# Kernel tuning notes

Measured on AMD Instinct MI355X. Metric: run time of the kernel, lower is better.

The kernel has to match this reference:

```python
import jax, jax.numpy as jnp
import numpy as np

B, C, H, W = 16, 384, 56, 56
NH, WS, SS = 12, 7, 3          # num_heads, window_size, shift_size
MLP = 4 * C
N = WS * WS                     # tokens per window (49)
nHW = H // WS                   # windows per side (8)
nW = nHW * nHW                  # windows per image (64)
HD = C // NH                    # head dim (32)
EPS = 1e-5


def _ln(x, g, b):
    mu = jnp.mean(x, axis=-1, keepdims=True)
    var = jnp.mean(jnp.square(x - mu), axis=-1, keepdims=True)
    return (x - mu) * jax.lax.rsqrt(var + EPS) * g + b


def _attn_mask():
    # static shifted-window mask, computed once with numpy (constants)
    img = np.zeros((H, W))
    sl = (slice(0, -WS), slice(-WS, -SS), slice(-SS, None))
    cnt = 0
    for hs in sl:
        for ws_ in sl:
            img[hs, ws_] = cnt
            cnt += 1
    mw = img.reshape(nHW, WS, nHW, WS).transpose(0, 2, 1, 3).reshape(-1, N)
    d = mw[:, None, :] - mw[:, :, None]          # (nW, N, N)
    return jnp.asarray(np.where(d != 0, -100.0, 0.0), jnp.float32)

_MASK = _attn_mask()


def setup_inputs() -> dict:
    key = jax.random.key(0)
    ks = jax.random.split(key, 6)
    rn = lambda k, s: jax.random.normal(k, s, jnp.float32) * 0.02
    return {
        "x": jax.random.normal(ks[0], (B, C, H, W), jnp.float32),
        "norm1_g": jnp.ones((C,), jnp.float32),
        "norm1_b": jnp.zeros((C,), jnp.float32),
        "qkv_w": rn(ks[1], (C, 3 * C)),
        "qkv_b": jnp.zeros((3 * C,), jnp.float32),
        "proj_w": rn(ks[2], (C, C)),
        "proj_b": jnp.zeros((C,), jnp.float32),
        "norm2_g": jnp.ones((C,), jnp.float32),
        "norm2_b": jnp.zeros((C,), jnp.float32),
        "fc1_w": rn(ks[3], (C, MLP)),
        "fc1_b": jnp.zeros((MLP,), jnp.float32),
        "fc2_w": rn(ks[4], (MLP, C)),
        "fc2_b": jnp.zeros((C,), jnp.float32),
    }


def reference(x, norm1_g, norm1_b, qkv_w, qkv_b, proj_w, proj_b,
              norm2_g, norm2_b, fc1_w, fc1_b, fc2_w, fc2_b):
    shortcut = x                                   # (B, C, H, W)
    xh = jnp.transpose(x, (0, 2, 3, 1))            # (B, H, W, C)
    xh = _ln(xh, norm1_g, norm1_b)
    # H, W divisible by WS -> padding is a no-op; shifted window path
    xs = jnp.roll(xh, (-SS, -SS), axis=(1, 2))
    # window partition -> (B*nW, N, C)
    xw = xs.reshape(B, nHW, WS, nHW, WS, C).transpose(0, 1, 3, 2, 4, 5)
    xw = xw.reshape(-1, N, C)
    # attention
    qkv = (xw @ qkv_w + qkv_b).reshape(-1, N, 3, NH, HD).transpose(2, 0, 3, 1, 4)
    q, k, v = qkv[0] * HD ** -0.5, qkv[1], qkv[2]  # (B*nW, NH, N, HD)
    attn = jnp.einsum('whnd,whmd->whnm', q, k)     # (B*nW, NH, N, N)
    attn = attn.reshape(B, nW, NH, N, N) + _MASK[None, :, None]
    attn = jax.nn.softmax(attn, axis=-1).reshape(-1, NH, N, N)
    out = jnp.einsum('whnm,whmd->whnd', attn, v)   # (B*nW, NH, N, HD)
    out = out.transpose(0, 2, 1, 3).reshape(-1, N, C)
    out = out @ proj_w + proj_b
    # window reverse -> (B, H, W, C), un-shift
    xs = out.reshape(B, nHW, nHW, WS, WS, C).transpose(0, 1, 3, 2, 4, 5)
    xs = xs.reshape(B, H, W, C)
    xh = jnp.roll(xs, (SS, SS), axis=(1, 2))
    x2 = shortcut + jnp.transpose(xh, (0, 3, 1, 2))
    # MLP residual (in BHWC)
    xh2 = jnp.transpose(x2, (0, 2, 3, 1))
    h = jax.nn.gelu(_ln(xh2, norm2_g, norm2_b) @ fc1_w + fc1_b,
                    approximate=False) @ fc2_w + fc2_b
    xh2 = xh2 + h
    return jnp.transpose(xh2, (0, 3, 1, 2))
```

## Files before the change

### kernel.cpp

```cpp
#include <hip/hip_runtime.h>
#include <hip/hip_bf16.h>
#include <math.h>
#include <stdint.h>

#define C_ 384
#define TOKENS 50176

typedef __bf16 bf16;
typedef __bf16 bf16x8 __attribute__((ext_vector_type(8)));
typedef __bf16 bf16x4 __attribute__((ext_vector_type(4)));
typedef float  f32x4  __attribute__((ext_vector_type(4)));

__device__ __forceinline__ float b2f(bf16 x) { return (float)x; }
__device__ __forceinline__ bf16  f2b(float x) { return (bf16)x; }

__device__ __forceinline__ float fast_gelu(float v) {
    float u2 = v * fmaf(v * v, 0.07135481f, 1.5957691f);
    return v / (1.0f + __expf(-u2));
}

__device__ __forceinline__ void gld_lds16(const bf16* g, bf16* l) {
    __builtin_amdgcn_global_load_lds(
        (const __attribute__((address_space(1))) void*)g,
        (__attribute__((address_space(3))) void*)l, 16, 0, 0);
}

#define SB() __builtin_amdgcn_sched_barrier(0)
#define SYNC_FENCE() do { __builtin_amdgcn_sched_barrier(0); \
                          __builtin_amdgcn_s_barrier(); \
                          __builtin_amdgcn_sched_barrier(0); } while (0)
#define WAITVM(N) do { asm volatile("s_waitcnt vmcnt(" #N ")" ::: "memory"); SB(); } while (0)
#define WAITLG()  do { asm volatile("s_waitcnt lgkmcnt(0)" ::: "memory"); SB(); } while (0)

__global__ void wtrans_kernel(const float* __restrict__ in, bf16* __restrict__ out,
                              int K, int N) {
    int idx = blockIdx.x * 256 + threadIdx.x;
    if (idx >= K * N) return;
    int n = idx / K, k = idx % K;
    out[idx] = f2b(in[(size_t)k * N + n]);
}

__global__ __launch_bounds__(256) void ln1_gather_kernel(
    const float* __restrict__ x, const float* __restrict__ g,
    const float* __restrict__ bt, bf16* __restrict__ xw) {
    int wave = threadIdx.x >> 6, lane = threadIdx.x & 63;
    int T = blockIdx.x * 4 + wave;
    int wi = T / 49, n = T % 49;
    int b = wi >> 6, w64 = wi & 63;
    int bh = w64 >> 3, bw = w64 & 7;
    int hs = bh * 7 + n / 7 + 3; if (hs >= 56) hs -= 56;
    int wsd = bw * 7 + n % 7 + 3; if (wsd >= 56) wsd -= 56;
    const float* xp = x + (size_t)b * C_ * 3136 + hs * 56 + wsd;
    float v[6];
    #pragma unroll
    for (int k = 0; k < 6; k++) v[k] = xp[(size_t)(lane + k * 64) * 3136];
    float s = v[0] + v[1] + v[2] + v[3] + v[4] + v[5];
    #pragma unroll
    for (int m = 32; m; m >>= 1) s += __shfl_xor(s, m);
    float mu = s * (1.0f / 384.0f);
    float s2 = 0.f;
    #pragma unroll
    for (int k = 0; k < 6; k++) { float d = v[k] - mu; s2 += d * d; }
    #pragma unroll
    for (int m = 32; m; m >>= 1) s2 += __shfl_xor(s2, m);
    float rstd = rsqrtf(s2 * (1.0f / 384.0f) + 1e-5f);
    bf16* op = xw + (size_t)T * 384;
    #pragma unroll
    for (int k = 0; k < 6; k++) {
        int c = lane + k * 64;
        op[c] = f2b((v[k] - mu) * rstd * g[c] + bt[c]);
    }
}

enum { EPI_NONE = 0, EPI_GELU = 1, EPI_PROJ = 2, EPI_FC2 = 3 };


__device__ __forceinline__ void ldg_a2(f32x4& d0, f32x4& d1, const bf16* p) {
    asm volatile("global_load_dwordx4 %0, %2, off\n\t"
                 "global_load_dwordx4 %1, %2, off offset:64"
                 : "=&v"(d0), "=&v"(d1) : "v"(p) : "memory");
}

__device__ __forceinline__ void stage_B(const bf16* const (&gB)[4], bf16* Bsb,
                                        int t, int k0) {
    #pragma unroll
    for (int p = 0; p < 4; p++) gld_lds16(gB[p] + k0, Bsb + (p * 256 + t) * 8);
}

#define LDA(A0, A1)                                                     \
    do {                                                                \
        _Pragma("unroll")                                               \
        for (int i_ = 0; i_ < 4; i_++) ldg_a2(A0[i_], A1[i_], ga[i_]);  \
        _Pragma("unroll")                                               \
        for (int i_ = 0; i_ < 4; i_++) ga[i_] += 64;                    \
    } while (0)

#define RDB(Bsb)                                                              \
    do {                                                                      \
        const char* Bb_ = (const char*)(Bsb);                                 \
        _Pragma("unroll")                                                     \
        for (int j_ = 0; j_ < 4; j_++)                                        \
            b0[j_] = *(const bf16x8*)(Bb_ + bB + j_ * 2048);                  \
        _Pragma("unroll")                                                     \
        for (int j_ = 0; j_ < 4; j_++)                                        \
            b1[j_] = *(const bf16x8*)(Bb_ + (bB ^ 64) + j_ * 2048);           \
    } while (0)

#define MMAC(A0, A1)                                                           \
    do {                                                                       \
        __builtin_amdgcn_s_setprio(1);                                         \
        _Pragma("unroll")                                                      \
        for (int j_ = 0; j_ < 4; j_++)                                         \
            _Pragma("unroll")                                                  \
            for (int i_ = 0; i_ < 4; i_++)                                     \
                acc[j_][i_] = __builtin_amdgcn_mfma_f32_16x16x32_bf16(         \
                    b0[j_], __builtin_bit_cast(bf16x8, A0[i_]), acc[j_][i_],   \
                    0, 0, 0);                                                  \
        _Pragma("unroll")                                                      \
        for (int j_ = 0; j_ < 4; j_++)                                         \
            _Pragma("unroll")                                                  \
            for (int i_ = 0; i_ < 4; i_++)                                     \
                acc[j_][i_] = __builtin_amdgcn_mfma_f32_16x16x32_bf16(         \
                    b1[j_], __builtin_bit_cast(bf16x8, A1[i_]), acc[j_][i_],   \
                    0, 0, 0);                                                  \
        __builtin_amdgcn_s_setprio(0);                                         \
        __builtin_amdgcn_sched_barrier(0);                                     \
    } while (0)

template <int EPI>
__global__ __launch_bounds__(256, 2) void gemm_kernel(
    const bf16* __restrict__ A, const bf16* __restrict__ Wt,
    const float* __restrict__ bias, bf16* __restrict__ Cout,
    int Kdim, int Ndim,
    const float* __restrict__ resx,
    const bf16* __restrict__ resb) {
    __shared__ __align__(16) bf16 Bs[2][128 * 64];
    int t = threadIdx.x;

    int nwg = gridDim.x * gridDim.y;
    int bid = blockIdx.y * gridDim.x + blockIdx.x;
    int q8 = nwg >> 3, r8 = nwg & 7, xcd = bid & 7, off = bid >> 3;
    int swz = (xcd < r8 ? xcd * (q8 + 1) : r8 * (q8 + 1) + (xcd - r8) * q8) + off;
    int n0 = (swz % gridDim.x) * 128;
    int m0 = (swz / gridDim.x) * 128;

    int lane = t & 63, wave = t >> 6;
    int wr = wave >> 1, wc = wave & 1;
    int quad = lane >> 4, lm = lane & 15;
    f32x4 acc[4][4] = {};

    const bf16* gB[4];
    #pragma unroll
    for (int p = 0; p < 4; p++) {
        int idx = p * 256 + t;
        int row = idx >> 3, g = idx & 7;
        int gs = g ^ (row & 7);
        gB[p] = Wt + (size_t)(n0 + row) * Kdim + gs * 8;
    }
    int g0 = quad ^ (lm & 7);
    int bB = ((wc * 64 + lm) * 64 + g0 * 8) * 2;

    const bf16* ga[4];
    #pragma unroll
    for (int i = 0; i < 4; i++)
        ga[i] = A + (size_t)(m0 + wr * 64 + i * 16 + lm) * Kdim + quad * 8;

    f32x4 aE0[4], aE1[4], aO0[4], aO1[4];
    bf16x8 b0[4], b1[4];

    int nt = Kdim >> 6;
    stage_B(gB, Bs[0], t, 0);
    stage_B(gB, Bs[1], t, 64);
    LDA(aE0, aE1);
    WAITVM(0);
    SYNC_FENCE();

    for (int tk = 0; tk < nt; tk += 2) {
        RDB(Bs[0]);
        LDA(aO0, aO1);
        WAITVM(12);
        WAITLG();
        MMAC(aE0, aE1);
        SYNC_FENCE();
        if (tk + 2 < nt) {
            stage_B(gB, Bs[0], t, (tk + 2) << 6);
            WAITVM(12);
        } else {
            WAITVM(8);
        }
        SYNC_FENCE();
        RDB(Bs[1]);
        if (tk + 2 < nt) {
            LDA(aE0, aE1);
            WAITVM(12);
        } else {
            WAITVM(0);
        }
        WAITLG();
        MMAC(aO0, aO1);
        if (tk + 2 < nt) {
            SYNC_FENCE();
            stage_B(gB, Bs[1], t, (tk + 3) << 6);
            WAITVM(12);
            SYNC_FENCE();
        }
    }

    #pragma unroll
    for (int i = 0; i < 4; i++) {
        int m = m0 + wr * 64 + i * 16 + lm;
        size_t resbase = 0;
        if (EPI == EPI_PROJ) {
            int wi = m / 49, n_ = m % 49;
            int b = wi >> 6, w64 = wi & 63;
            int bh = w64 >> 3, bw = w64 & 7;
            int hs = bh * 7 + n_ / 7 + 3; if (hs >= 56) hs -= 56;
            int wsd = bw * 7 + n_ % 7 + 3; if (wsd >= 56) wsd -= 56;
            resbase = (size_t)b * C_ * 3136 + hs * 56 + wsd;
        }
        #pragma unroll
        for (int j = 0; j < 4; j++) {
            int nb = n0 + wc * 64 + j * 16 + quad * 4;
            f32x4 bj = *(const f32x4*)(bias + nb);
            f32x4 v;
            #pragma unroll
            for (int r = 0; r < 4; r++) v[r] = acc[j][i][r] + bj[r];
            if (EPI == EPI_GELU) {
                #pragma unroll
                for (int r = 0; r < 4; r++) v[r] = fast_gelu(v[r]);
            }
            if (EPI == EPI_PROJ) {
                #pragma unroll
                for (int r = 0; r < 4; r++) v[r] += resx[resbase + (size_t)(nb + r) * 3136];
            }
            if (EPI == EPI_FC2) {
                bf16x4 rb = *(const bf16x4*)(resb + (size_t)m * 384 + nb);
                #pragma unroll
                for (int r = 0; r < 4; r++) v[r] += b2f(rb[r]);
            }
            bf16x4 o;
            #pragma unroll
            for (int r = 0; r < 4; r++) o[r] = f2b(v[r]);
            *(bf16x4*)(Cout + (size_t)m * Ndim + nb) = o;
        }
    }
}

__global__ __launch_bounds__(64) void attn_mfma_kernel(const bf16* __restrict__ qkv,
                                                       bf16* __restrict__ aout) {
    __shared__ __align__(16) bf16 pbuf[64 * 72];
    __shared__ int reg_[64];
    int l = threadIdx.x;
    int wi = blockIdx.x / 12, h = blockIdx.x % 12;
    int i16 = l & 15, quad = l >> 4;

    {
        int tok = l < 49 ? l : 48;
        int w64 = wi & 63;
        int bh = w64 >> 3, bw = w64 & 7;
        int hh = bh * 7 + tok / 7, ww = bw * 7 + tok % 7;
        int fh = hh < 49 ? 0 : (hh < 53 ? 1 : 2);
        int fw = ww < 49 ? 0 : (ww < 53 ? 1 : 2);
        reg_[l] = fh * 3 + fw;
    }
    __syncthreads();

    const bf16* qbase = qkv + (size_t)wi * 49 * 1152 + h * 32;

    f32x4 s_[4][4] = {};
    bf16x8 af[4], bfr[4];
    #pragma unroll
    for (int mi = 0; mi < 4; mi++) {
        int m = mi * 16 + i16; if (m > 48) m = 48;
        af[mi] = *(const bf16x8*)(qbase + (size_t)m * 1152 + quad * 8);
    }
    #pragma unroll
    for (int nt = 0; nt < 4; nt++) {
        int n = nt * 16 + i16; if (n > 48) n = 48;
        bfr[nt] = *(const bf16x8*)(qbase + 384 + (size_t)n * 1152 + quad * 8);
    }
    #pragma unroll
    for (int mi = 0; mi < 4; mi++)
        #pragma unroll
        for (int nt = 0; nt < 4; nt++)
            s_[mi][nt] = __builtin_amdgcn_mfma_f32_16x16x32_bf16(af[mi], bfr[nt], s_[mi][nt], 0, 0, 0);

    int creg[4];
    #pragma unroll
    for (int nt = 0; nt < 4; nt++) {
        int c = nt * 16 + i16; if (c > 48) c = 48;
        creg[nt] = reg_[c];
    }

    const float scale = 0.17677669529663687f;
    #pragma unroll
    for (int mi = 0; mi < 4; mi++) {
        #pragma unroll
        for (int r = 0; r < 4; r++) {
            int row = mi * 16 + quad * 4 + r;
            int rreg = reg_[row];
            float v[4]; float mx = -1e30f;
            #pragma unroll
            for (int nt = 0; nt < 4; nt++) {
                int c = nt * 16 + i16;
                float x = s_[mi][nt][r] * scale;
                if (c > 48) x = -1e30f;
                else if (rreg != creg[nt]) x -= 100.0f;
                v[nt] = x; mx = fmaxf(mx, x);
            }
            #pragma unroll
            for (int m = 8; m; m >>= 1) mx = fmaxf(mx, __shfl_xor(mx, m));
            float sum = 0.f;
            #pragma unroll
            for (int nt = 0; nt < 4; nt++) { v[nt] = __expf(v[nt] - mx); sum += v[nt]; }
            #pragma unroll
            for (int m = 8; m; m >>= 1) sum += __shfl_xor(sum, m);
            float inv = 1.0f / sum;
            #pragma unroll
            for (int nt = 0; nt < 4; nt++)
                pbuf[row * 72 + nt * 16 + i16] = f2b(v[nt] * inv);
        }
    }
    __syncthreads();

    f32x4 o_[4][2] = {};
    const bf16* vbase = qkv + (size_t)wi * 49 * 1152 + 768 + h * 32;
    #pragma unroll
    for (int ks = 0; ks < 2; ks++) {
        bf16x8 pa[4];
        #pragma unroll
        for (int mi = 0; mi < 4; mi++)
            pa[mi] = *(const bf16x8*)(pbuf + (mi * 16 + i16) * 72 + ks * 32 + quad * 8);
        bf16x8 vb[2];
        #pragma unroll
        for (int nt = 0; nt < 2; nt++)
            #pragma unroll
            for (int j = 0; j < 8; j++) {
                int tok = ks * 32 + quad * 8 + j; if (tok > 48) tok = 48;
                vb[nt][j] = vbase[(size_t)tok * 1152 + nt * 16 + i16];
            }
        #pragma unroll
        for (int mi = 0; mi < 4; mi++)
            #pragma unroll
            for (int nt = 0; nt < 2; nt++)
                o_[mi][nt] = __builtin_amdgcn_mfma_f32_16x16x32_bf16(pa[mi], vb[nt], o_[mi][nt], 0, 0, 0);
    }

    bf16* obase = aout + (size_t)wi * 49 * 384 + h * 32;
    #pragma unroll
    for (int mi = 0; mi < 4; mi++)
        #pragma unroll
        for (int r = 0; r < 4; r++) {
            int row = mi * 16 + quad * 4 + r;
            if (row < 49) {
                #pragma unroll
                for (int nt = 0; nt < 2; nt++)
                    obase[(size_t)row * 384 + nt * 16 + i16] = f2b(o_[mi][nt][r]);
            }
        }
}

__global__ __launch_bounds__(256) void ln2_kernel(const bf16* __restrict__ x2,
                                                  const float* __restrict__ g,
                                                  const float* __restrict__ bt,
                                                  bf16* __restrict__ x2n) {
    int wave = threadIdx.x >> 6, lane = threadIdx.x & 63;
    int T = blockIdx.x * 4 + wave;
    const bf16* xp = x2 + (size_t)T * 384;
    float v[6];
    #pragma unroll
    for (int k = 0; k < 6; k++) v[k] = b2f(xp[lane + k * 64]);
    float s = v[0] + v[1] + v[2] + v[3] + v[4] + v[5];
    #pragma unroll
    for (int m = 32; m; m >>= 1) s += __shfl_xor(s, m);
    float mu = s * (1.0f / 384.0f);
    float s2 = 0.f;
    #pragma unroll
    for (int k = 0; k < 6; k++) { float d = v[k] - mu; s2 += d * d; }
    #pragma unroll
    for (int m = 32; m; m >>= 1) s2 += __shfl_xor(s2, m);
    float rstd = rsqrtf(s2 * (1.0f / 384.0f) + 1e-5f);
    bf16* op = x2n + (size_t)T * 384;
    #pragma unroll
    for (int k = 0; k < 6; k++) {
        int c = lane + k * 64;
        op[c] = f2b((v[k] - mu) * rstd * g[c] + bt[c]);
    }
}

__global__ __launch_bounds__(256) void untile_kernel(const bf16* __restrict__ otok,
                                                     float* __restrict__ out) {
    __shared__ float tile[56 * 65];
    int t = threadIdx.x;
    int b = blockIdx.x / 336;
    int rem = blockIdx.x % 336;
    int h = rem / 6;
    int c0 = (rem % 6) * 64;
    int hs = h + 53; if (hs >= 56) hs -= 56;
    int bh = hs / 7, th = hs % 7;
    #pragma unroll
    for (int pass = 0; pass < 14; pass++) {
        int w = pass * 4 + (t >> 6);
        int c = t & 63;
        int wsd = w + 53; if (wsd >= 56) wsd -= 56;
        int T = (b * 64 + bh * 8 + wsd / 7) * 49 + th * 7 + wsd % 7;
        tile[w * 65 + c] = b2f(otok[(size_t)T * 384 + c0 + c]);
    }
    __syncthreads();
    #pragma unroll
    for (int pass = 0; pass < 14; pass++) {
        int idx = pass * 256 + t;
        int c = idx / 56, w = idx % 56;
        out[((size_t)(b * 384 + c0 + c)) * 3136 + h * 56 + w] = tile[w * 65 + c];
    }
}

extern "C" void kernel_launch(void* const* d_in, const int* in_sizes, int n_in,
                              void* d_out, int out_size, void* d_ws, size_t ws_size,
                              hipStream_t stream) {
    (void)in_sizes; (void)n_in; (void)out_size; (void)ws_size;
    const float* x      = (const float*)d_in[0];
    const float* n1g    = (const float*)d_in[1];
    const float* n1b    = (const float*)d_in[2];
    const float* qkv_w  = (const float*)d_in[3];
    const float* qkv_b  = (const float*)d_in[4];
    const float* proj_w = (const float*)d_in[5];
    const float* proj_b = (const float*)d_in[6];
    const float* n2g    = (const float*)d_in[7];
    const float* n2b    = (const float*)d_in[8];
    const float* fc1_w  = (const float*)d_in[9];
    const float* fc1_b  = (const float*)d_in[10];
    const float* fc2_w  = (const float*)d_in[11];
    const float* fc2_b  = (const float*)d_in[12];
    float* out = (float*)d_out;
    char* ws = (char*)d_ws;

    bf16* qkv_wT = (bf16*)(ws + 0);
    bf16* proj_wT = (bf16*)(ws + 884736);
    bf16* fc1_wT = (bf16*)(ws + 1179648);
    bf16* fc2_wT = (bf16*)(ws + 2359296);
    bf16* xw   = (bf16*)(ws + 4194304);
    bf16* qkvb = (bf16*)(ws + 42729472);
    bf16* attn = (bf16*)(ws + 158334976);
    bf16* x2   = (bf16*)(ws + 4194304);
    bf16* x2n  = (bf16*)(ws + 42729472);
    bf16* h1   = (bf16*)(ws + 81264640);
    bf16* otok = (bf16*)(ws + 235405312);

    wtrans_kernel<<<(384 * 1152 + 255) / 256, 256, 0, stream>>>(qkv_w, qkv_wT, 384, 1152);
    wtrans_kernel<<<(384 * 384 + 255) / 256, 256, 0, stream>>>(proj_w, proj_wT, 384, 384);
    wtrans_kernel<<<(384 * 1536 + 255) / 256, 256, 0, stream>>>(fc1_w, fc1_wT, 384, 1536);
    wtrans_kernel<<<(1536 * 384 + 255) / 256, 256, 0, stream>>>(fc2_w, fc2_wT, 1536, 384);

    ln1_gather_kernel<<<TOKENS / 4, 256, 0, stream>>>(x, n1g, n1b, xw);

    gemm_kernel<EPI_NONE><<<dim3(9, 392), 256, 0, stream>>>(
        xw, qkv_wT, qkv_b, qkvb, 384, 1152, nullptr, nullptr);

    attn_mfma_kernel<<<12288, 64, 0, stream>>>(qkvb, attn);

    gemm_kernel<EPI_PROJ><<<dim3(3, 392), 256, 0, stream>>>(
        attn, proj_wT, proj_b, x2, 384, 384, x, nullptr);

    ln2_kernel<<<TOKENS / 4, 256, 0, stream>>>(x2, n2g, n2b, x2n);

    gemm_kernel<EPI_GELU><<<dim3(12, 392), 256, 0, stream>>>(
        x2n, fc1_wT, fc1_b, h1, 384, 1536, nullptr, nullptr);

    gemm_kernel<EPI_FC2><<<dim3(3, 392), 256, 0, stream>>>(
        h1, fc2_wT, fc2_b, otok, 1536, 384, nullptr, x2);

    untile_kernel<<<16 * 336, 256, 0, stream>>>(otok, out);
}
```

Baseline: 794.6 us.

## Preload full K weight panel into LDS and double M tile per block

The GEMM kernel now uses 512 threads and a 256-row M tile. For K=384 GEMMs it loads the entire 128x384 weight panel into LDS once with an XOR swizzle and drops the per-iteration double-buffered staging and its barriers. For the K=1536 FC2 GEMM it skips LDS entirely and streams B fragments directly from global memory into registers. This is meant to remove LDS sync overhead and improve reuse, at the cost of 96KB LDS per block (which may limit occupancy) and more register pressure.

Result: slower. 956.0 us (+20.3%).

```diff
diff --git a/kernel.cpp b/kernel.cpp
--- a/kernel.cpp
+++ b/kernel.cpp
@@ -75,35 +75,46 @@
 enum { EPI_NONE = 0, EPI_GELU = 1, EPI_PROJ = 2, EPI_FC2 = 3 };
 
 
-__device__ __forceinline__ void ldg_a2(f32x4& d0, f32x4& d1, const bf16* p) {
+__device__ __forceinline__ void ldg2(f32x4& d0, f32x4& d1, const bf16* p) {
     asm volatile("global_load_dwordx4 %0, %2, off\n\t"
                  "global_load_dwordx4 %1, %2, off offset:64"
                  : "=&v"(d0), "=&v"(d1) : "v"(p) : "memory");
 }
 
-__device__ __forceinline__ void stage_B(const bf16* const (&gB)[4], bf16* Bsb,
-                                        int t, int k0) {
-    #pragma unroll
-    for (int p = 0; p < 4; p++) gld_lds16(gB[p] + k0, Bsb + (p * 256 + t) * 8);
-}
-
 #define LDA(A0, A1)                                                     \
     do {                                                                \
         _Pragma("unroll")                                               \
-        for (int i_ = 0; i_ < 4; i_++) ldg_a2(A0[i_], A1[i_], ga[i_]);  \
+        for (int i_ = 0; i_ < 4; i_++) ldg2(A0[i_], A1[i_], ga[i_]);    \
         _Pragma("unroll")                                               \
         for (int i_ = 0; i_ < 4; i_++) ga[i_] += 64;                    \
     } while (0)
 
-#define RDB(Bsb)                                                              \
+#define LDB(B0, B1)                                                     \
+    do {                                                                \
+        _Pragma("unroll")                                               \
+        for (int j_ = 0; j_ < 4; j_++) ldg2(B0[j_], B1[j_], gb[j_]);    \
+        _Pragma("unroll")                                               \
+        for (int j_ = 0; j_ < 4; j_++) gb[j_] += 64;                    \
+    } while (0)
+
+#define RDBL(TK)                                                              \
     do {                                                                      \
-        const char* Bb_ = (const char*)(Bsb);                                 \
+        const char* wb_ = (const char*)Ws + (TK) * 128;                       \
         _Pragma("unroll")                                                     \
         for (int j_ = 0; j_ < 4; j_++)                                        \
-            b0[j_] = *(const bf16x8*)(Bb_ + bB + j_ * 2048);                  \
+            b0[j_] = *(const bf16x8*)(wb_ + bB + j_ * 12288);                 \
         _Pragma("unroll")                                                     \
         for (int j_ = 0; j_ < 4; j_++)                                        \
-            b1[j_] = *(const bf16x8*)(Bb_ + (bB ^ 64) + j_ * 2048);           \
+            b1[j_] = *(const bf16x8*)(wb_ + (bB ^ 64) + j_ * 12288);          \
+    } while (0)
+
+#define CVTB(BS0, BS1)                                                        \
+    do {                                                                      \
+        _Pragma("unroll")                                                     \
+        for (int j_ = 0; j_ < 4; j_++) {                                      \
+            b0[j_] = __builtin_bit_cast(bf16x8, BS0[j_]);                     \
+            b1[j_] = __builtin_bit_cast(bf16x8, BS1[j_]);                     \
+        }                                                                     \
     } while (0)
 
 #define MMAC(A0, A1)                                                           \
@@ -127,14 +138,14 @@
         __builtin_amdgcn_sched_barrier(0);                                     \
     } while (0)
 
-template <int EPI>
-__global__ __launch_bounds__(256, 2) void gemm_kernel(
+template <int EPI, bool BLDS>
+__global__ __launch_bounds__(512, 2) void gemm_kernel(
     const bf16* __restrict__ A, const bf16* __restrict__ Wt,
     const float* __restrict__ bias, bf16* __restrict__ Cout,
     int Kdim, int Ndim,
     const float* __restrict__ resx,
     const bf16* __restrict__ resb) {
-    __shared__ __align__(16) bf16 Bs[2][128 * 64];
+    __shared__ __align__(16) bf16 Ws[BLDS ? 128 * 384 : 8];
     int t = threadIdx.x;
 
     int nwg = gridDim.x * gridDim.y;
@@ -142,68 +153,75 @@
     int q8 = nwg >> 3, r8 = nwg & 7, xcd = bid & 7, off = bid >> 3;
     int swz = (xcd < r8 ? xcd * (q8 + 1) : r8 * (q8 + 1) + (xcd - r8) * q8) + off;
     int n0 = (swz % gridDim.x) * 128;
-    int m0 = (swz / gridDim.x) * 128;
+    int m0 = (swz / gridDim.x) * 256;
 
     int lane = t & 63, wave = t >> 6;
     int wr = wave >> 1, wc = wave & 1;
     int quad = lane >> 4, lm = lane & 15;
     f32x4 acc[4][4] = {};
 
-    const bf16* gB[4];
-    #pragma unroll
-    for (int p = 0; p < 4; p++) {
-        int idx = p * 256 + t;
-        int row = idx >> 3, g = idx & 7;
-        int gs = g ^ (row & 7);
-        gB[p] = Wt + (size_t)(n0 + row) * Kdim + gs * 8;
-    }
-    int g0 = quad ^ (lm & 7);
-    int bB = ((wc * 64 + lm) * 64 + g0 * 8) * 2;
+    if (BLDS) {
+        #pragma unroll
+        for (int q = 0; q < 12; q++) {
+            int idx = q * 512 + t;
+            int row = idx / 48, cg = idx % 48;
+            int sg = (cg & ~7) | ((cg & 7) ^ (row & 7));
+            gld_lds16(Wt + (size_t)(n0 + row) * 384 + sg * 8, Ws + idx * 8);
+        }
+    }
 
     const bf16* ga[4];
     #pragma unroll
     for (int i = 0; i < 4; i++)
         ga[i] = A + (size_t)(m0 + wr * 64 + i * 16 + lm) * Kdim + quad * 8;
+    const bf16* gb[4];
+    if (!BLDS) {
+        #pragma unroll
+        for (int j = 0; j < 4; j++)
+            gb[j] = Wt + (size_t)(n0 + wc * 64 + j * 16 + lm) * Kdim + quad * 8;
+    }
+    int bB = (wc * 64 + lm) * 768 + (quad ^ (lm & 7)) * 16;
 
     f32x4 aE0[4], aE1[4], aO0[4], aO1[4];
+    f32x4 bE0[4], bE1[4], bO0[4], bO1[4];
     bf16x8 b0[4], b1[4];
 
     int nt = Kdim >> 6;
-    stage_B(gB, Bs[0], t, 0);
-    stage_B(gB, Bs[1], t, 64);
     LDA(aE0, aE1);
-    WAITVM(0);
-    SYNC_FENCE();
+    if (!BLDS) {
+        LDB(bE0, bE1);
+    } else {
+        WAITVM(0);
+        SYNC_FENCE();
+    }
 
     for (int tk = 0; tk < nt; tk += 2) {
-        RDB(Bs[0]);
+        if (BLDS) RDBL(tk);
         LDA(aO0, aO1);
-        WAITVM(12);
-        WAITLG();
-        MMAC(aE0, aE1);
-        SYNC_FENCE();
-        if (tk + 2 < nt) {
-            stage_B(gB, Bs[0], t, (tk + 2) << 6);
-            WAITVM(12);
+        if (!BLDS) {
+            LDB(bO0, bO1);
+            WAITVM(16);
+            CVTB(bE0, bE1);
         } else {
             WAITVM(8);
-        }
-        SYNC_FENCE();
-        RDB(Bs[1]);
+            WAITLG();
+        }
+        MMAC(aE0, aE1);
+        if (BLDS) RDBL(tk + 1);
         if (tk + 2 < nt) {
             LDA(aE0, aE1);
-            WAITVM(12);
+            if (!BLDS) {
+                LDB(bE0, bE1);
+                WAITVM(16);
+            } else {
+                WAITVM(8);
+            }
         } else {
             WAITVM(0);
         }
-        WAITLG();
+        if (!BLDS) CVTB(bO0, bO1);
+        else WAITLG();
         MMAC(aO0, aO1);
-        if (tk + 2 < nt) {
-            SYNC_FENCE();
-            stage_B(gB, Bs[1], t, (tk + 3) << 6);
-            WAITVM(12);
-            SYNC_FENCE();
-        }
     }
 
     #pragma unroll
@@ -454,20 +472,20 @@
 
     ln1_gather_kernel<<<TOKENS / 4, 256, 0, stream>>>(x, n1g, n1b, xw);
 
-    gemm_kernel<EPI_NONE><<<dim3(9, 392), 256, 0, stream>>>(
+    gemm_kernel<EPI_NONE, true><<<dim3(9, 196), 512, 0, stream>>>(
         xw, qkv_wT, qkv_b, qkvb, 384, 1152, nullptr, nullptr);
 
     attn_mfma_kernel<<<12288, 64, 0, stream>>>(qkvb, attn);
 
-    gemm_kernel<EPI_PROJ><<<dim3(3, 392), 256, 0, stream>>>(
+    gemm_kernel<EPI_PROJ, true><<<dim3(3, 196), 512, 0, stream>>>(
         attn, proj_wT, proj_b, x2, 384, 384, x, nullptr);
 
     ln2_kernel<<<TOKENS / 4, 256, 0, stream>>>(x2, n2g, n2b, x2n);
 
-    gemm_kernel<EPI_GELU><<<dim3(12, 392), 256, 0, stream>>>(
+    gemm_kernel<EPI_GELU, true><<<dim3(12, 196), 512, 0, stream>>>(
         x2n, fc1_wT, fc1_b, h1, 384, 1536, nullptr, nullptr);
 
-    gemm_kernel<EPI_FC2><<<dim3(3, 392), 256, 0, stream>>>(
+    gemm_kernel<EPI_FC2, false><<<dim3(3, 196), 512, 0, stream>>>(
         h1, fc2_wT, fc2_b, otok, 1536, 384, nullptr, x2);
 
     untile_kernel<<<16 * 336, 256, 0, stream>>>(otok, out);
```
